# Kernel optimization log

Hardware: AMD Instinct MI355X
Metric: run time of the kernel (lower is better)

Reference implementation:

```python
import jax, jax.numpy as jnp
import numpy as np

NH = 8        # num_heads
SH = 1        # sub_heads
TD = 4        # transition_dim
ID = 512      # input_dim
FACTOR = 0.1  # orthogonalization_factor
ORDER = 16    # orthogonalization_order
EPS = 1e-3
EIG_FACTOR = 1.0
B, S = 4, 4096


def ortho_exp(lmat):
    """matrix_orthogonalize_exponential: exp(skew(A)) via truncated power series."""
    shape = lmat.shape
    X = shape[-1]
    mat = lmat.reshape(-1, X, X)
    mat_skew = FACTOR * (mat - jnp.swapaxes(mat, -2, -1))
    mat_max = jnp.sqrt(jnp.sum(mat_skew ** 2 + EPS, axis=(-2, -1), keepdims=True))
    normalizer = jnp.maximum(mat_max, jnp.ones_like(mat_max))
    sk = mat_skew / normalizer
    eye = jnp.broadcast_to(jnp.eye(X, dtype=lmat.dtype), sk.shape)
    powers = [eye]
    for _ in range(ORDER - 1):
        powers.append(jnp.matmul(powers[-1], sk))
    powers = jnp.stack(powers, axis=0)  # [order, N, X, X]
    orange = jnp.arange(ORDER, dtype=lmat.dtype)
    lognorm = jnp.cumsum(jnp.where(orange > 0, jnp.log(orange), 0.0))
    # coeff[o, n] = normalizer_n**o / o!
    coeff = jnp.exp(jnp.log(normalizer.reshape(-1))[None, :] * orange[:, None] - lognorm[:, None])
    exp_mat = jnp.einsum('on,onxy->nxy', coeff, powers)
    return exp_mat.reshape(shape)


def setup_inputs() -> dict:
    key = jax.random.key(0)
    ks = jax.random.split(key, 7)
    x = jax.random.normal(ks[0], (B, S, ID), dtype=jnp.float32)
    inproj_bias = 0.02 * jax.random.normal(ks[1], (NH, TD, TD), dtype=jnp.float32)
    inproj_weight = 0.02 * jax.random.normal(ks[2], (NH // SH, SH, TD, TD, ID // SH), dtype=jnp.float32)
    outproj_bias = 0.02 * jax.random.normal(ks[3], (NH, TD, TD), dtype=jnp.float32)
    outproj_weight = 0.02 * jax.random.normal(ks[4], (NH // SH, SH, TD, TD, ID // SH), dtype=jnp.float32)
    eigenvalues_bias = jax.random.normal(ks[5], (NH, TD), dtype=jnp.float32)
    eigenvalues_weight = 0.02 * jax.random.normal(ks[6], (NH // SH, SH, TD, ID // SH), dtype=jnp.float32)
    return dict(x=x, inproj_bias=inproj_bias, inproj_weight=inproj_weight,
                outproj_bias=outproj_bias, outproj_weight=outproj_weight,
                eigenvalues_bias=eigenvalues_bias, eigenvalues_weight=eigenvalues_weight)


def reference(x, inproj_bias, inproj_weight, outproj_bias, outproj_weight,
              eigenvalues_bias, eigenvalues_weight):
    b, s, d = x.shape
    xr = x.reshape(b, s, SH, d // SH)
    # eigenvalues: [B,S,NH,TD]
    eig = eigenvalues_bias + jnp.einsum('nsbc,...sc->...nsb', eigenvalues_weight, xr).reshape(b, s, NH, TD)
    eig_act = jnp.tanh(EIG_FACTOR * eig)
    # input/output projection matrices: [B,S,NH,TD,TD]
    in_pre = inproj_bias + jnp.einsum('nsbcd,...sd->...nsbc', inproj_weight, xr).reshape(b, s, NH, TD, TD)
    in_mat = ortho_exp(in_pre)
    out_pre = outproj_bias + jnp.einsum('nsbcd,...sd->...nsbc', outproj_weight, xr).reshape(b, s, NH, TD, TD)
    out_mat = ortho_exp(out_pre)
    # transition = out_mat @ diag(eig_act) @ in_mat
    transition = jnp.einsum('...nab,...nb,...nbc->...nac', out_mat, eig_act, in_mat)
    return transition
```

## Files before the change

kernel.cpp:

```cpp
#include <hip/hip_runtime.h>
#include <math.h>

typedef __attribute__((ext_vector_type(8))) short short8;
typedef __attribute__((ext_vector_type(16))) float f32x16;

namespace {
constexpr int kID = 512;
constexpr int kNO = 288;
constexpr int kBM = 64;
constexpr int kNT = 9;
constexpr int kKS = 32;
constexpr int kCS = 296;
constexpr float kFactor = 0.1f;
}

__device__ __forceinline__ unsigned short f2bf(float f) {
    unsigned u = __float_as_uint(f);
    unsigned r = 0x7fffu + ((u >> 16) & 1u);
    return (unsigned short)((u + r) >> 16);
}

__global__ void prep_w(const float* __restrict__ inW, const float* __restrict__ outW,
                       const float* __restrict__ eigW, unsigned short* __restrict__ wws) {
    int gid = blockIdx.x * 256 + threadIdx.x;
    if (gid >= kKS * kNT * 64) return;
    int lane  = gid & 63;
    int nt    = (gid >> 6) % kNT;
    int kstep = gid / (64 * kNT);
    int n = nt * 32 + (lane & 31);
    int k = kstep * 16 + (lane >> 5) * 8;
    const float* src = (n < 128 ? inW + (size_t)n * kID
                       : n < 256 ? outW + (size_t)(n - 128) * kID
                                 : eigW + (size_t)(n - 256) * kID) + k;
    unsigned short* dst = wws + (size_t)gid * 8;
    #pragma unroll
    for (int j = 0; j < 8; ++j) dst[j] = f2bf(src[j]);
}

__global__ __launch_bounds__(384)
void lrt_main(const float* __restrict__ x, const unsigned short* __restrict__ wws,
              const float* __restrict__ inB, const float* __restrict__ outB,
              const float* __restrict__ eigB, float* __restrict__ out) {
    __shared__ float Cld[32 * kCS];
    __shared__ float sB[kNO];

    const int tid  = threadIdx.x;
    const int tok0 = blockIdx.x * kBM;

    if (tid < kNO)
        sB[tid] = tid < 128 ? inB[tid] : tid < 256 ? outB[tid - 128] : eigB[tid - 256];

    const int w    = tid >> 6;
    const int lane = tid & 63;
    const int mt   = w & 1;
    const int ng   = w >> 1;
    const int row  = mt * 32 + (lane & 31);
    const int h    = lane >> 5;

    f32x16 acc0, acc1, acc2;
    #pragma unroll
    for (int i = 0; i < 16; ++i) { acc0[i] = 0.f; acc1[i] = 0.f; acc2[i] = 0.f; }

    const float* xrow = x + (size_t)(tok0 + row) * kID + h * 8;
    const uint4* wp = (const uint4*)wws;
    const int bcol = ng * 3;

    #pragma unroll 4
    for (int ks = 0; ks < kKS; ++ks) {
        float4 a0 = *(const float4*)(xrow + ks * 16);
        float4 a1 = *(const float4*)(xrow + ks * 16 + 4);
        short8 a;
        a[0] = (short)f2bf(a0.x); a[1] = (short)f2bf(a0.y);
        a[2] = (short)f2bf(a0.z); a[3] = (short)f2bf(a0.w);
        a[4] = (short)f2bf(a1.x); a[5] = (short)f2bf(a1.y);
        a[6] = (short)f2bf(a1.z); a[7] = (short)f2bf(a1.w);

        uint4 b0 = wp[(size_t)((ks * kNT + bcol + 0) * 64 + lane)];
        uint4 b1 = wp[(size_t)((ks * kNT + bcol + 1) * 64 + lane)];
        uint4 b2 = wp[(size_t)((ks * kNT + bcol + 2) * 64 + lane)];

        acc0 = __builtin_amdgcn_mfma_f32_32x32x16_bf16(a, __builtin_bit_cast(short8, b0), acc0, 0, 0, 0);
        acc1 = __builtin_amdgcn_mfma_f32_32x32x16_bf16(a, __builtin_bit_cast(short8, b1), acc1, 0, 0, 0);
        acc2 = __builtin_amdgcn_mfma_f32_32x32x16_bf16(a, __builtin_bit_cast(short8, b2), acc2, 0, 0, 0);
    }

    for (int hf = 0; hf < 2; ++hf) {
        __syncthreads();
        if (mt == hf) {
            #pragma unroll
            for (int i = 0; i < 3; ++i) {
                const f32x16& A = (i == 0) ? acc0 : (i == 1) ? acc1 : acc2;
                const int col = (bcol + i) * 32 + (lane & 31);
                #pragma unroll
                for (int rg = 0; rg < 16; ++rg) {
                    int trow = (rg & 3) + 8 * (rg >> 2) + 4 * h;
                    Cld[trow * kCS + col] = A[rg];
                }
            }
        }
        __syncthreads();
        if (tid < 256) {
            const int t = tid >> 3, head = tid & 7;
            const float* cr = &Cld[t * kCS];

            float Min[16], Mout[16], d[4];
            #pragma unroll
            for (int i = 0; i < 16; ++i) Min[i]  = cr[head * 16 + i]       + sB[head * 16 + i];
            #pragma unroll
            for (int i = 0; i < 16; ++i) Mout[i] = cr[128 + head * 16 + i] + sB[128 + head * 16 + i];
            #pragma unroll
            for (int b = 0; b < 4; ++b)  d[b] = tanhf(cr[256 + head * 4 + b] + sB[256 + head * 4 + b]);

            float Ein[16], Eout[16];
            #pragma unroll
            for (int side = 0; side < 2; ++side) {
                const float* M = side ? Mout : Min;
                float S[16];
                #pragma unroll
                for (int a = 0; a < 4; ++a)
                    #pragma unroll
                    for (int b = 0; b < 4; ++b)
                        S[a * 4 + b] = kFactor * (M[a * 4 + b] - M[b * 4 + a]);
                float R[16];
                #pragma unroll
                for (int i = 0; i < 16; ++i) R[i] = (i % 5 == 0) ? 1.0f : 0.0f;
                #pragma unroll
                for (int j = 15; j >= 1; --j) {
                    const float inv = 1.0f / (float)j;
                    float Rn[16];
                    #pragma unroll
                    for (int a = 0; a < 4; ++a)
                        #pragma unroll
                        for (int c = 0; c < 4; ++c) {
                            float s = S[a * 4 + 0] * R[0 * 4 + c];
                            s = fmaf(S[a * 4 + 1], R[1 * 4 + c], s);
                            s = fmaf(S[a * 4 + 2], R[2 * 4 + c], s);
                            s = fmaf(S[a * 4 + 3], R[3 * 4 + c], s);
                            Rn[a * 4 + c] = s * inv + ((a == c) ? 1.0f : 0.0f);
                        }
                    #pragma unroll
                    for (int i = 0; i < 16; ++i) R[i] = Rn[i];
                }
                float* E = side ? Eout : Ein;
                #pragma unroll
                for (int i = 0; i < 16; ++i) E[i] = R[i];
            }

            float R[16];
            #pragma unroll
            for (int a = 0; a < 4; ++a) {
                float od0 = Eout[a * 4 + 0] * d[0];
                float od1 = Eout[a * 4 + 1] * d[1];
                float od2 = Eout[a * 4 + 2] * d[2];
                float od3 = Eout[a * 4 + 3] * d[3];
                #pragma unroll
                for (int c = 0; c < 4; ++c) {
                    float s = od0 * Ein[0 * 4 + c];
                    s = fmaf(od1, Ein[1 * 4 + c], s);
                    s = fmaf(od2, Ein[2 * 4 + c], s);
                    s = fmaf(od3, Ein[3 * 4 + c], s);
                    R[a * 4 + c] = s;
                }
            }

            float* op = out + ((size_t)(tok0 + hf * 32 + t) * 8 + head) * 16;
            #pragma unroll
            for (int a = 0; a < 4; ++a)
                *(float4*)(op + a * 4) = make_float4(R[a * 4 + 0], R[a * 4 + 1],
                                                     R[a * 4 + 2], R[a * 4 + 3]);
        }
    }
}

extern "C" void kernel_launch(void* const* d_in, const int* in_sizes, int n_in,
                              void* d_out, int out_size, void* d_ws, size_t ws_size,
                              hipStream_t stream) {
    const float* x    = (const float*)d_in[0];
    const float* inB  = (const float*)d_in[1];
    const float* inW  = (const float*)d_in[2];
    const float* outB = (const float*)d_in[3];
    const float* outW = (const float*)d_in[4];
    const float* eigB = (const float*)d_in[5];
    const float* eigW = (const float*)d_in[6];
    float* out = (float*)d_out;

    unsigned short* wws = (unsigned short*)d_ws;

    const int n_tokens = in_sizes[0] / kID;
    const int n_blocks = n_tokens / kBM;

    prep_w<<<(kKS * kNT * 64 + 255) / 256, 256, 0, stream>>>(inW, outW, eigW, wws);
    lrt_main<<<n_blocks, 384, 0, stream>>>(x, wws, inB, outB, eigB, out);
}
```

Measured before the change: 111.0 us.

## Halve token tile, stage bf16 x in swizzled LDS, parallelize exponentials across sides

The token tile shrinks from 64 to 32, giving twice as many blocks, and each block now runs 9 waves, one per output N tile. The x tile is converted to bf16 once and staged in XOR-swizzled shared memory that aliases the C buffer, so it is no longer reloaded by every wave. The two matrix exponentials per head are now computed by separate threads (512 active instead of 256) and written back to LDS before a final combine pass. This adds an extra barrier and more blocks, and it relies on higher occupancy through the 576-thread launch bound with 5 blocks per CU.

```diff
diff --git a/kernel.cpp b/kernel.cpp
--- a/kernel.cpp
+++ b/kernel.cpp
@@ -7,11 +7,14 @@
 namespace {
 constexpr int kID = 512;
 constexpr int kNO = 288;
-constexpr int kBM = 64;
+constexpr int kBM = 32;
 constexpr int kNT = 9;
 constexpr int kKS = 32;
 constexpr int kCS = 296;
 constexpr float kFactor = 0.1f;
+constexpr int kABytes = kKS * 1024;
+constexpr int kCBytes = kBM * kCS * 4;
+constexpr int kSmem   = kCBytes + kNO * 4;
 }
 
 __device__ __forceinline__ unsigned short f2bf(float f) {
@@ -37,12 +40,14 @@
     for (int j = 0; j < 8; ++j) dst[j] = f2bf(src[j]);
 }
 
-__global__ __launch_bounds__(384)
+__global__ __launch_bounds__(576, 5)
 void lrt_main(const float* __restrict__ x, const unsigned short* __restrict__ wws,
               const float* __restrict__ inB, const float* __restrict__ outB,
               const float* __restrict__ eigB, float* __restrict__ out) {
-    __shared__ float Cld[32 * kCS];
-    __shared__ float sB[kNO];
+    __shared__ __align__(16) char smem[kSmem];
+    char*  Ash = smem;
+    float* Cld = (float*)smem;
+    float* sB  = (float*)(smem + kCBytes);
 
     const int tid  = threadIdx.x;
     const int tok0 = blockIdx.x * kBM;
@@ -50,125 +55,134 @@
     if (tid < kNO)
         sB[tid] = tid < 128 ? inB[tid] : tid < 256 ? outB[tid - 128] : eigB[tid - 256];
 
-    const int w    = tid >> 6;
+    for (int j = tid; j < kBM * 64; j += 576) {
+        const int t  = j >> 6;
+        const int k8 = j & 63;
+        const float* src = x + (size_t)(tok0 + t) * kID + k8 * 8;
+        float4 v0 = *(const float4*)(src);
+        float4 v1 = *(const float4*)(src + 4);
+        short8 a;
+        a[0] = (short)f2bf(v0.x); a[1] = (short)f2bf(v0.y);
+        a[2] = (short)f2bf(v0.z); a[3] = (short)f2bf(v0.w);
+        a[4] = (short)f2bf(v1.x); a[5] = (short)f2bf(v1.y);
+        a[6] = (short)f2bf(v1.z); a[7] = (short)f2bf(v1.w);
+        const int ks = k8 >> 1, h = k8 & 1;
+        int byte = ks * 1024 + (t + 32 * h) * 16;
+        byte ^= (ks & 7) << 4;
+        *(short8*)(Ash + byte) = a;
+    }
+    __syncthreads();
+
+    const int wv   = tid >> 6;
     const int lane = tid & 63;
-    const int mt   = w & 1;
-    const int ng   = w >> 1;
-    const int row  = mt * 32 + (lane & 31);
-    const int h    = lane >> 5;
-
-    f32x16 acc0, acc1, acc2;
+    f32x16 acc;
     #pragma unroll
-    for (int i = 0; i < 16; ++i) { acc0[i] = 0.f; acc1[i] = 0.f; acc2[i] = 0.f; }
-
-    const float* xrow = x + (size_t)(tok0 + row) * kID + h * 8;
+    for (int i = 0; i < 16; ++i) acc[i] = 0.f;
+
     const uint4* wp = (const uint4*)wws;
-    const int bcol = ng * 3;
-
-    #pragma unroll 4
+    #pragma unroll 8
     for (int ks = 0; ks < kKS; ++ks) {
-        float4 a0 = *(const float4*)(xrow + ks * 16);
-        float4 a1 = *(const float4*)(xrow + ks * 16 + 4);
-        short8 a;
-        a[0] = (short)f2bf(a0.x); a[1] = (short)f2bf(a0.y);
-        a[2] = (short)f2bf(a0.z); a[3] = (short)f2bf(a0.w);
-        a[4] = (short)f2bf(a1.x); a[5] = (short)f2bf(a1.y);
-        a[6] = (short)f2bf(a1.z); a[7] = (short)f2bf(a1.w);
-
-        uint4 b0 = wp[(size_t)((ks * kNT + bcol + 0) * 64 + lane)];
-        uint4 b1 = wp[(size_t)((ks * kNT + bcol + 1) * 64 + lane)];
-        uint4 b2 = wp[(size_t)((ks * kNT + bcol + 2) * 64 + lane)];
-
-        acc0 = __builtin_amdgcn_mfma_f32_32x32x16_bf16(a, __builtin_bit_cast(short8, b0), acc0, 0, 0, 0);
-        acc1 = __builtin_amdgcn_mfma_f32_32x32x16_bf16(a, __builtin_bit_cast(short8, b1), acc1, 0, 0, 0);
-        acc2 = __builtin_amdgcn_mfma_f32_32x32x16_bf16(a, __builtin_bit_cast(short8, b2), acc2, 0, 0, 0);
-    }
-
-    for (int hf = 0; hf < 2; ++hf) {
-        __syncthreads();
-        if (mt == hf) {
-            #pragma unroll
-            for (int i = 0; i < 3; ++i) {
-                const f32x16& A = (i == 0) ? acc0 : (i == 1) ? acc1 : acc2;
-                const int col = (bcol + i) * 32 + (lane & 31);
-                #pragma unroll
-                for (int rg = 0; rg < 16; ++rg) {
-                    int trow = (rg & 3) + 8 * (rg >> 2) + 4 * h;
-                    Cld[trow * kCS + col] = A[rg];
-                }
-            }
-        }
-        __syncthreads();
-        if (tid < 256) {
-            const int t = tid >> 3, head = tid & 7;
-            const float* cr = &Cld[t * kCS];
-
-            float Min[16], Mout[16], d[4];
-            #pragma unroll
-            for (int i = 0; i < 16; ++i) Min[i]  = cr[head * 16 + i]       + sB[head * 16 + i];
-            #pragma unroll
-            for (int i = 0; i < 16; ++i) Mout[i] = cr[128 + head * 16 + i] + sB[128 + head * 16 + i];
-            #pragma unroll
-            for (int b = 0; b < 4; ++b)  d[b] = tanhf(cr[256 + head * 4 + b] + sB[256 + head * 4 + b]);
-
-            float Ein[16], Eout[16];
-            #pragma unroll
-            for (int side = 0; side < 2; ++side) {
-                const float* M = side ? Mout : Min;
-                float S[16];
-                #pragma unroll
-                for (int a = 0; a < 4; ++a)
-                    #pragma unroll
-                    for (int b = 0; b < 4; ++b)
-                        S[a * 4 + b] = kFactor * (M[a * 4 + b] - M[b * 4 + a]);
-                float R[16];
-                #pragma unroll
-                for (int i = 0; i < 16; ++i) R[i] = (i % 5 == 0) ? 1.0f : 0.0f;
-                #pragma unroll
-                for (int j = 15; j >= 1; --j) {
-                    const float inv = 1.0f / (float)j;
-                    float Rn[16];
-                    #pragma unroll
-                    for (int a = 0; a < 4; ++a)
-                        #pragma unroll
-                        for (int c = 0; c < 4; ++c) {
-                            float s = S[a * 4 + 0] * R[0 * 4 + c];
-                            s = fmaf(S[a * 4 + 1], R[1 * 4 + c], s);
-                            s = fmaf(S[a * 4 + 2], R[2 * 4 + c], s);
-                            s = fmaf(S[a * 4 + 3], R[3 * 4 + c], s);
-                            Rn[a * 4 + c] = s * inv + ((a == c) ? 1.0f : 0.0f);
-                        }
-                    #pragma unroll
-                    for (int i = 0; i < 16; ++i) R[i] = Rn[i];
-                }
-                float* E = side ? Eout : Ein;
-                #pragma unroll
-                for (int i = 0; i < 16; ++i) E[i] = R[i];
-            }
-
-            float R[16];
-            #pragma unroll
-            for (int a = 0; a < 4; ++a) {
-                float od0 = Eout[a * 4 + 0] * d[0];
-                float od1 = Eout[a * 4 + 1] * d[1];
-                float od2 = Eout[a * 4 + 2] * d[2];
-                float od3 = Eout[a * 4 + 3] * d[3];
+        int byte = (ks * 1024 + lane * 16) ^ ((ks & 7) << 4);
+        short8 a = *(const short8*)(Ash + byte);
+        uint4  b = wp[(size_t)((ks * kNT + wv) * 64 + lane)];
+        acc = __builtin_amdgcn_mfma_f32_32x32x16_bf16(a, __builtin_bit_cast(short8, b), acc, 0, 0, 0);
+    }
+    __syncthreads();
+
+    {
+        const int col = wv * 32 + (lane & 31);
+        const int h   = lane >> 5;
+        #pragma unroll
+        for (int rg = 0; rg < 16; ++rg) {
+            int trow = (rg & 3) + 8 * (rg >> 2) + 4 * h;
+            Cld[trow * kCS + col] = acc[rg];
+        }
+    }
+    __syncthreads();
+
+    if (tid < 512) {
+        const int side = tid & 1, head = (tid >> 1) & 7, t = tid >> 4;
+        float* cr = Cld + t * kCS + side * 128 + head * 16;
+        const float* bb = sB + side * 128 + head * 16;
+
+        float M[16];
+        #pragma unroll
+        for (int c = 0; c < 4; ++c) {
+            float4 v = *(const float4*)(cr + c * 4);
+            M[c * 4 + 0] = v.x + bb[c * 4 + 0];
+            M[c * 4 + 1] = v.y + bb[c * 4 + 1];
+            M[c * 4 + 2] = v.z + bb[c * 4 + 2];
+            M[c * 4 + 3] = v.w + bb[c * 4 + 3];
+        }
+        float S[16];
+        #pragma unroll
+        for (int a = 0; a < 4; ++a)
+            #pragma unroll
+            for (int b = 0; b < 4; ++b)
+                S[a * 4 + b] = kFactor * (M[a * 4 + b] - M[b * 4 + a]);
+
+        float R[16];
+        #pragma unroll
+        for (int i = 0; i < 16; ++i) R[i] = (i % 5 == 0) ? 1.0f : 0.0f;
+        #pragma unroll
+        for (int j = 15; j >= 1; --j) {
+            const float inv = 1.0f / (float)j;
+            float Rn[16];
+            #pragma unroll
+            for (int a = 0; a < 4; ++a)
                 #pragma unroll
                 for (int c = 0; c < 4; ++c) {
-                    float s = od0 * Ein[0 * 4 + c];
-                    s = fmaf(od1, Ein[1 * 4 + c], s);
-                    s = fmaf(od2, Ein[2 * 4 + c], s);
-                    s = fmaf(od3, Ein[3 * 4 + c], s);
-                    R[a * 4 + c] = s;
+                    float s = S[a * 4 + 0] * R[0 * 4 + c];
+                    s = fmaf(S[a * 4 + 1], R[1 * 4 + c], s);
+                    s = fmaf(S[a * 4 + 2], R[2 * 4 + c], s);
+                    s = fmaf(S[a * 4 + 3], R[3 * 4 + c], s);
+                    Rn[a * 4 + c] = s * inv + ((a == c) ? 1.0f : 0.0f);
                 }
+            #pragma unroll
+            for (int i = 0; i < 16; ++i) R[i] = Rn[i];
+        }
+        #pragma unroll
+        for (int c = 0; c < 4; ++c)
+            *(float4*)(cr + c * 4) = make_float4(R[c * 4 + 0], R[c * 4 + 1],
+                                                 R[c * 4 + 2], R[c * 4 + 3]);
+    }
+    __syncthreads();
+
+    if (tid < 256) {
+        const int t = tid >> 3, head = tid & 7;
+        const float* cr = Cld + t * kCS;
+
+        float Ein[16], Eout[16], d[4];
+        #pragma unroll
+        for (int i = 0; i < 16; ++i) Ein[i]  = cr[head * 16 + i];
+        #pragma unroll
+        for (int i = 0; i < 16; ++i) Eout[i] = cr[128 + head * 16 + i];
+        #pragma unroll
+        for (int b = 0; b < 4; ++b)
+            d[b] = tanhf(cr[256 + head * 4 + b] + sB[256 + head * 4 + b]);
+
+        float R[16];
+        #pragma unroll
+        for (int a = 0; a < 4; ++a) {
+            float od0 = Eout[a * 4 + 0] * d[0];
+            float od1 = Eout[a * 4 + 1] * d[1];
+            float od2 = Eout[a * 4 + 2] * d[2];
+            float od3 = Eout[a * 4 + 3] * d[3];
+            #pragma unroll
+            for (int c = 0; c < 4; ++c) {
+                float s = od0 * Ein[0 * 4 + c];
+                s = fmaf(od1, Ein[1 * 4 + c], s);
+                s = fmaf(od2, Ein[2 * 4 + c], s);
+                s = fmaf(od3, Ein[3 * 4 + c], s);
+                R[a * 4 + c] = s;
             }
-
-            float* op = out + ((size_t)(tok0 + hf * 32 + t) * 8 + head) * 16;
-            #pragma unroll
-            for (int a = 0; a < 4; ++a)
-                *(float4*)(op + a * 4) = make_float4(R[a * 4 + 0], R[a * 4 + 1],
-                                                     R[a * 4 + 2], R[a * 4 + 3]);
-        }
+        }
+
+        float* op = out + ((size_t)(tok0 + t) * 8 + head) * 16;
+        #pragma unroll
+        for (int a = 0; a < 4; ++a)
+            *(float4*)(op + a * 4) = make_float4(R[a * 4 + 0], R[a * 4 + 1],
+                                                 R[a * 4 + 2], R[a * 4 + 3]);
     }
 }
 
@@ -190,5 +204,5 @@
     const int n_blocks = n_tokens / kBM;
 
     prep_w<<<(kKS * kNT * 64 + 255) / 256, 256, 0, stream>>>(inW, outW, eigW, wws);
-    lrt_main<<<n_blocks, 384, 0, stream>>>(x, wws, inB, outB, eigB, out);
-}
+    lrt_main<<<n_blocks, 576, 0, stream>>>(x, wws, inB, outB, eigB, out);
+}
```

New measurement: 100.7 us. -9.3%, faster.
